# Kernel tuning notes

Hardware: AMD Instinct MI355X
Metric: run time of the kernel (lower is better)

Reference implementation:

```python
import math
import jax, jax.numpy as jnp
import numpy as np

EPS = 1e-5  # torch LayerNorm default
K_MA = 25   # moving-average kernel


def _layernorm(x, g, b):
    mu = x.mean(-1, keepdims=True)
    var = ((x - mu) ** 2).mean(-1, keepdims=True)
    return (x - mu) * jax.lax.rsqrt(var + EPS) * g + b


def _moving_avg(x, k=K_MA):
    # x: [B, L, C]; edge-replicate pad (k-1)//2 on both sides, avg window k, stride 1
    pad = (k - 1) // 2
    front = jnp.repeat(x[:, :1], pad, axis=1)
    back = jnp.repeat(x[:, -1:], pad, axis=1)
    xp = jnp.concatenate([front, x, back], axis=1)          # [B, L+2*pad, C]
    cs = jnp.cumsum(xp, axis=1)
    cs = jnp.concatenate([jnp.zeros_like(cs[:, :1]), cs], axis=1)
    return (cs[:, k:] - cs[:, :-k]) / k                     # [B, L, C]


def _autocorrelation(q, k, v, factor=1):
    # q,k,v: [B, L, H, D] -> FFT cross-correlation along time, top-k lag aggregation (inference path)
    B, L, H, D = q.shape
    qp = q.transpose(0, 2, 3, 1)                            # [B,H,D,L]
    kp = k.transpose(0, 2, 3, 1)
    vp = v.transpose(0, 2, 3, 1)
    qf = jnp.fft.rfft(qp, axis=-1)
    kf = jnp.fft.rfft(kp, axis=-1)
    corr = jnp.fft.irfft(qf * jnp.conj(kf), n=L, axis=-1)   # [B,H,D,L]

    top_k = int(factor * math.log(L))
    mean_corr = corr.mean(axis=(1, 2))                      # [B,L]
    weights, delay = jax.lax.top_k(mean_corr, top_k)        # [B,k]
    alpha = jax.nn.softmax(weights, axis=-1)                # [B,k]

    base = jnp.arange(L)
    agg = jnp.zeros_like(vp)
    for i in range(top_k):  # small static loop (top_k = 7)
        idx = (base[None, :] + delay[:, i:i + 1]) % L       # circular gather == roll by -delay
        gathered = jnp.take_along_axis(vp, idx[:, None, None, :], axis=-1)
        agg = agg + gathered * alpha[:, i][:, None, None, None]
    return agg.transpose(0, 3, 1, 2)                        # [B,L,H,D]


def _forward(x, Wq, Wk, Wv, Wo, bo, ln_g, ln_b, W1, W2, num_heads=16, factor=1):
    B, L, C = x.shape
    H = num_heads
    D = C // H
    xn = _layernorm(x, ln_g, ln_b)
    q = jnp.einsum('blc,oc->blo', xn, Wq).reshape(B, L, H, D)
    k = jnp.einsum('blc,oc->blo', xn, Wk).reshape(B, L, H, D)
    v = jnp.einsum('blc,oc->blo', xn, Wv).reshape(B, L, H, D)
    agg = _autocorrelation(q, k, v, factor=factor).reshape(B, L, C)
    attn_out = jnp.einsum('blc,oc->blo', agg, Wo) + bo
    x = x + attn_out
    x = x - _moving_avg(x)                                  # decomp1 seasonal part
    # FFN: 1x1 convs == linear layers, exact GELU (torch default)
    y = jax.nn.gelu(jnp.einsum('blc,hc->blh', x, W1), approximate=False)
    y = jnp.einsum('blh,ch->blc', y, W2)
    x = x + y
    x = x - _moving_avg(x)                                  # decomp2 seasonal part
    return x


def setup_inputs() -> dict:
    key = jax.random.key(0)
    ks = jax.random.split(key, 8)
    B, L, C = 8, 2048, 1024
    Hd = 4 * C
    s = 0.02
    return {
        'x': jax.random.normal(ks[0], (B, L, C), dtype=jnp.float32),
        'Wq': jax.random.normal(ks[1], (C, C), dtype=jnp.float32) * s,
        'Wk': jax.random.normal(ks[2], (C, C), dtype=jnp.float32) * s,
        'Wv': jax.random.normal(ks[3], (C, C), dtype=jnp.float32) * s,
        'Wo': jax.random.normal(ks[4], (C, C), dtype=jnp.float32) * s,
        'bo': jnp.zeros((C,), dtype=jnp.float32),
        'ln_g': jnp.ones((C,), dtype=jnp.float32),
        'ln_b': jnp.zeros((C,), dtype=jnp.float32),
        'W1': jax.random.normal(ks[5], (Hd, C), dtype=jnp.float32) * s,
        'W2': jax.random.normal(ks[6], (C, Hd), dtype=jnp.float32) * s,
    }


def reference(x, Wq, Wk, Wv, Wo, bo, ln_g, ln_b, W1, W2):
    return _forward(x, Wq, Wk, Wv, Wo, bo, ln_g, ln_b, W1, W2)
```

## Files before the change

kernel.cpp:

```cpp
#include <hip/hip_runtime.h>
#include <cstdint>
#include <cstddef>


typedef _Float16 half8 __attribute__((ext_vector_type(8)));
typedef _Float16 half4 __attribute__((ext_vector_type(4)));
typedef float floatx4 __attribute__((ext_vector_type(4)));

#define PI_F 3.14159265358979323846f
#define ZP32(i) ((i) + ((i) >> 5))

__device__ __forceinline__ void load_lds16(const void* g, void* l) {
  __builtin_amdgcn_global_load_lds((__attribute__((address_space(1))) void*)g,
                                   (__attribute__((address_space(3))) void*)l,
                                   16, 0, 0);
}

__device__ __forceinline__ float fast_gelu(float v) {
  float u = v * 0.70710678118654752f;
  float au = fabsf(u);
  float t = __builtin_amdgcn_rcpf(1.0f + 0.3275911f * au);
  float poly = t * (0.254829592f +
               t * (-0.284496736f +
               t * (1.421413741f +
               t * (-1.453152027f +
               t * 1.061405429f))));
  float e = __expf(-u * u);
  float erf_abs = 1.0f - poly * e;
  float erfv = copysignf(erf_abs, u);
  return 0.5f * v * (1.0f + erfv);
}


__global__ __launch_bounds__(256) void cvt_f16_kernel(const float* __restrict__ src,
                                                      _Float16* __restrict__ dst, int n4) {
  int i = blockIdx.x * 256 + threadIdx.x;
  if (i >= n4) return;
  float4 v = ((const float4*)src)[i];
  half4 h = {(_Float16)v.x, (_Float16)v.y, (_Float16)v.z, (_Float16)v.w};
  ((half4*)dst)[i] = h;
}

__global__ __launch_bounds__(256) void transpose_f16_kernel(const float* __restrict__ src,
                                                            _Float16* __restrict__ dst, int n) {
  __shared__ float tile[64][65];
  int j0 = blockIdx.y * 64, c0 = blockIdx.x * 64;
  int tr = threadIdx.x >> 4;
  int tc = threadIdx.x & 15;
#pragma unroll
  for (int rr = 0; rr < 64; rr += 16) {
    float4 v = *(const float4*)(src + (size_t)(j0 + tr + rr) * n + c0 + tc * 4);
    tile[tr + rr][tc * 4 + 0] = v.x;
    tile[tr + rr][tc * 4 + 1] = v.y;
    tile[tr + rr][tc * 4 + 2] = v.z;
    tile[tr + rr][tc * 4 + 3] = v.w;
  }
  __syncthreads();
#pragma unroll
  for (int rr = 0; rr < 64; rr += 16) {
    int c = tr + rr;
    half4 h = {(_Float16)tile[tc * 4 + 0][c], (_Float16)tile[tc * 4 + 1][c],
               (_Float16)tile[tc * 4 + 2][c], (_Float16)tile[tc * 4 + 3][c]};
    *(half4*)(dst + (size_t)(c0 + c) * n + j0 + tc * 4) = h;
  }
}

__global__ __launch_bounds__(256) void ln_kernel(const float* __restrict__ x,
                                                 const float* __restrict__ g,
                                                 const float* __restrict__ b,
                                                 _Float16* __restrict__ xn, int C) {
  int row = blockIdx.x;
  int t = threadIdx.x;
  const float4* xr = (const float4*)(x + (size_t)row * C);
  float4 v = xr[t];
  float s = v.x + v.y + v.z + v.w;
  float s2 = v.x * v.x + v.y * v.y + v.z * v.z + v.w * v.w;
  for (int o = 32; o > 0; o >>= 1) {
    s += __shfl_down(s, o, 64);
    s2 += __shfl_down(s2, o, 64);
  }
  __shared__ float red[8];
  int wave = t >> 6, lane = t & 63;
  if (lane == 0) { red[wave] = s; red[4 + wave] = s2; }
  __syncthreads();
  __shared__ float stats[2];
  if (t == 0) {
    float ts = red[0] + red[1] + red[2] + red[3];
    float ts2 = red[4] + red[5] + red[6] + red[7];
    float mu = ts / (float)C;
    float var = ts2 / (float)C - mu * mu;
    stats[0] = mu;
    stats[1] = 1.0f / sqrtf(var + 1e-5f);
  }
  __syncthreads();
  float mu = stats[0], rs = stats[1];
  float4 gv = ((const float4*)g)[t];
  float4 bv = ((const float4*)b)[t];
  half4 h = {(_Float16)((v.x - mu) * rs * gv.x + bv.x),
             (_Float16)((v.y - mu) * rs * gv.y + bv.y),
             (_Float16)((v.z - mu) * rs * gv.z + bv.z),
             (_Float16)((v.w - mu) * rs * gv.w + bv.w)};
  ((half4*)(xn + (size_t)row * C))[t] = h;
}

template <int EPI>
__global__ __launch_bounds__(512, 2) void gemm256_kernel(
    const _Float16* __restrict__ A, const _Float16* __restrict__ Bw,
    int M, int N, int K, int lda, int ldb,
    float* __restrict__ outf, _Float16* __restrict__ outh,
    const float* __restrict__ bias, const float* __restrict__ res) {
  __shared__ _Float16 lds[2][2][256 * 64];

  int tid = threadIdx.x;
  int lane = tid & 63;
  int wave = tid >> 6;
  int wm = wave >> 2;
  int wn = wave & 3;
  int ln15 = lane & 15, q4 = lane >> 4;
  int l3 = lane >> 3, l7 = lane & 7;

  int nwg = gridDim.x, orig = blockIdx.x;
  int wg = ((nwg & 7) == 0) ? ((orig & 7) * (nwg >> 3) + (orig >> 3)) : orig;
  int nbn = N >> 8;
  size_t m0 = (size_t)(wg / nbn) << 8;
  size_t n0 = (size_t)(wg % nbn) << 8;

  int sg0 = (q4 ^ l7) << 3;
  int sg1 = ((q4 + 4) ^ l7) << 3;

  floatx4 acc[8][4] = {};

  const _Float16* srcA = A + (m0 + 8 * wave + l3) * (size_t)lda + (size_t)((l7 ^ l3) * 8);
  const _Float16* srcB = Bw + (n0 + 8 * wave + l3) * (size_t)ldb + (size_t)((l7 ^ l3) * 8);
  char* ldsA0 = (char*)&lds[0][0][0] + wave * 1024;
  char* ldsB0 = (char*)&lds[0][1][0] + wave * 1024;

  load_lds16(srcB, ldsB0);
  load_lds16(srcB + (size_t)64 * ldb, ldsB0 + 1 * 8192);
  load_lds16(srcB + (size_t)128 * ldb, ldsB0 + 2 * 8192);
  load_lds16(srcB + (size_t)192 * ldb, ldsB0 + 3 * 8192);
  load_lds16(srcA, ldsA0);
  load_lds16(srcA + (size_t)128 * lda, ldsA0 + 2 * 8192);
  load_lds16(srcA + (size_t)64 * lda, ldsA0 + 1 * 8192);
  load_lds16(srcA + (size_t)192 * lda, ldsA0 + 3 * 8192);
  asm volatile("s_waitcnt vmcnt(2)" ::: "memory");
  __builtin_amdgcn_s_barrier();
  __builtin_amdgcn_sched_barrier(0);

  int nk = K >> 6;
  half8 bf[4][2], aA[2][2];

#define RD_B() _Pragma("unroll") for (int ni = 0; ni < 4; ++ni) {      \
    const _Float16* p_ = cB + ((wn * 64 + ni * 16 + ln15) << 6);       \
    bf[ni][0] = *(const half8*)(p_ + sg0);                             \
    bf[ni][1] = *(const half8*)(p_ + sg1); }
#define RD_A(mi) { const _Float16* p_ = cA + ((wm * 128 + (mi) * 16 + ln15) << 6); \
    aA[(mi) & 1][0] = *(const half8*)(p_ + sg0);                                   \
    aA[(mi) & 1][1] = *(const half8*)(p_ + sg1); }
#define MM(mi) _Pragma("unroll") for (int ni = 0; ni < 4; ++ni) {      \
    acc[mi][ni] = __builtin_amdgcn_mfma_f32_16x16x32_f16(aA[(mi) & 1][0], bf[ni][0], acc[mi][ni], 0, 0, 0); \
    acc[mi][ni] = __builtin_amdgcn_mfma_f32_16x16x32_f16(aA[(mi) & 1][1], bf[ni][1], acc[mi][ni], 0, 0, 0); }

#define PH_MID()                                            \
    __builtin_amdgcn_s_barrier();                           \
    asm volatile("s_waitcnt lgkmcnt(0)" ::: "memory");      \
    __builtin_amdgcn_sched_barrier(0);                      \
    __builtin_amdgcn_s_setprio(1);
#define PH_END()                                            \
    __builtin_amdgcn_s_setprio(0);                          \
    __builtin_amdgcn_s_barrier();                           \
    __builtin_amdgcn_sched_barrier(0);

  for (int t = 0; t < nk; ++t) {
    int cur = t & 1;
    const _Float16* cA = &lds[cur][0][0];
    const _Float16* cB = &lds[cur][1][0];
    const _Float16* As = srcA + (size_t)(t + 1) * 64;
    const _Float16* Bs = srcB + (size_t)(t + 1) * 64;
    char* stA = ldsA0 + (cur ^ 1) * 65536;
    char* stB = ldsB0 + (cur ^ 1) * 65536;
    bool pf = (t + 1 < nk);

    RD_B();
    RD_A(0); RD_A(1);
    if (pf) {
      load_lds16(Bs, stB);
      load_lds16(Bs + (size_t)64 * ldb, stB + 1 * 8192);
      load_lds16(Bs + (size_t)128 * ldb, stB + 2 * 8192);
    }
    PH_MID();
    MM(0); MM(1);
    PH_END();
    RD_A(2); RD_A(3);
    if (pf) {
      load_lds16(Bs + (size_t)192 * ldb, stB + 3 * 8192);
      load_lds16(As, stA);
      load_lds16(As + (size_t)128 * lda, stA + 2 * 8192);
    }
    PH_MID();
    MM(2); MM(3);
    __builtin_amdgcn_s_setprio(0);
    if (pf) {
      asm volatile("s_waitcnt vmcnt(6)" ::: "memory");
    } else {
      asm volatile("s_waitcnt vmcnt(0)" ::: "memory");
    }
    __builtin_amdgcn_s_barrier();
    __builtin_amdgcn_sched_barrier(0);
    RD_A(4); RD_A(5);
    if (pf) {
      load_lds16(As + (size_t)64 * lda, stA + 1 * 8192);
    }
    PH_MID();
    MM(4); MM(5);
    PH_END();
    RD_A(6); RD_A(7);
    if (pf) {
      load_lds16(As + (size_t)192 * lda, stA + 3 * 8192);
    }
    PH_MID();
    MM(6); MM(7);
    __builtin_amdgcn_s_setprio(0);
    asm volatile("s_waitcnt vmcnt(2)" ::: "memory");
    __builtin_amdgcn_s_barrier();
    __builtin_amdgcn_sched_barrier(0);
  }
#undef RD_B
#undef RD_A
#undef MM
#undef PH_MID
#undef PH_END

#pragma unroll
  for (int mi = 0; mi < 8; ++mi) {
#pragma unroll
    for (int ni = 0; ni < 4; ++ni) {
      floatx4 a4 = acc[mi][ni];
      size_t rowb = m0 + wm * 128 + mi * 16 + q4 * 4;
      size_t col = n0 + wn * 64 + ni * 16 + ln15;
      if (EPI == 5) {
        size_t b = rowb >> 11, l0 = rowb & 2047;
        half4 h = {(_Float16)a4[0], (_Float16)a4[1], (_Float16)a4[2], (_Float16)a4[3]};
        *(half4*)(outh + (((size_t)b * N + col) << 11) + l0) = h;
      } else {
#pragma unroll
        for (int r = 0; r < 4; ++r) {
          size_t idx = (rowb + r) * (size_t)N + col;
          float v = a4[r];
          if (EPI == 1) {
            outf[idx] = v + bias[col] + res[idx];
          } else if (EPI == 2) {
            outh[idx] = (_Float16)fast_gelu(v);
          } else if (EPI == 6) {
            outh[idx] = (_Float16)(v + res[idx]);
          } else if (EPI == 7) {
            float prev = (float)outh[idx];
            outh[idx] = (_Float16)(v + prev);
          } else {
            outh[idx] = (_Float16)v;
          }
        }
      }
    }
  }
}


#define CBFLY(ch, ia, ib, wr, wi) {                      \
    float ax_ = z[ch][ia].x, ay_ = z[ch][ia].y;          \
    float bx_ = z[ch][ib].x, by_ = z[ch][ib].y;          \
    float dx_ = ax_ - bx_, dy_ = ay_ - by_;              \
    z[ch][ia].x = ax_ + bx_; z[ch][ia].y = ay_ + by_;    \
    z[ch][ib].x = dx_ * (wr) - dy_ * (wi);               \
    z[ch][ib].y = dx_ * (wi) + dy_ * (wr); }
#define BFLY2(ia, ib, m) { float2 w_ = twl[ZP32(m)];     \
    CBFLY(0, ia, ib, w_.x, w_.y) CBFLY(1, ia, ib, w_.x, w_.y) }

__global__ __launch_bounds__(256) void corr_fft_kernel(const _Float16* __restrict__ F,
                                                       float* __restrict__ S) {
  __shared__ float2 Zs[2][2112];
  __shared__ float2 twl[1056];
  int tid = threadIdx.x;
  int b = blockIdx.x >> 9;
  int c0 = (blockIdx.x & 511) << 1;
  const _Float16* qb = F + ((size_t)(b * 2048 + c0) << 11);
  const _Float16* kb = F + ((size_t)(b * 2048 + 1024 + c0) << 11);

  float2 z[2][8];
#pragma unroll
  for (int j = 0; j < 8; ++j) {
    int p = tid + 256 * j;
    z[0][j] = make_float2((float)qb[p], (float)kb[p]);
    z[1][j] = make_float2((float)qb[2048 + p], (float)kb[2048 + p]);
  }
  for (int m = tid; m < 1024; m += 256) {
    float sn, cs;
    __sincosf(-PI_F * (float)m / 1024.0f, &sn, &cs);
    twl[ZP32(m)] = make_float2(cs, sn);
  }
  __syncthreads();

  BFLY2(0, 4, tid)
  BFLY2(1, 5, tid + 256)
  BFLY2(2, 6, tid + 512)
  BFLY2(3, 7, tid + 768)
  { float2 wA = twl[ZP32(tid << 1)], wB = twl[ZP32((tid + 256) << 1)];
    CBFLY(0, 0, 2, wA.x, wA.y) CBFLY(1, 0, 2, wA.x, wA.y)
    CBFLY(0, 1, 3, wB.x, wB.y) CBFLY(1, 1, 3, wB.x, wB.y)
    CBFLY(0, 4, 6, wA.x, wA.y) CBFLY(1, 4, 6, wA.x, wA.y)
    CBFLY(0, 5, 7, wB.x, wB.y) CBFLY(1, 5, 7, wB.x, wB.y) }
  { float2 wA = twl[ZP32(tid << 2)];
    CBFLY(0, 0, 1, wA.x, wA.y) CBFLY(1, 0, 1, wA.x, wA.y)
    CBFLY(0, 2, 3, wA.x, wA.y) CBFLY(1, 2, 3, wA.x, wA.y)
    CBFLY(0, 4, 5, wA.x, wA.y) CBFLY(1, 4, 5, wA.x, wA.y)
    CBFLY(0, 6, 7, wA.x, wA.y) CBFLY(1, 6, 7, wA.x, wA.y) }

#pragma unroll
  for (int j = 0; j < 8; ++j) {
    int p = tid + 256 * j;
    Zs[0][ZP32(p)] = z[0][j];
    Zs[1][ZP32(p)] = z[1][j];
  }
  __syncthreads();
  int t5 = tid & 31, hi1 = (tid >> 5) << 8;
#pragma unroll
  for (int j = 0; j < 8; ++j) {
    int p = hi1 + t5 + 32 * j;
    z[0][j] = Zs[0][ZP32(p)];
    z[1][j] = Zs[1][ZP32(p)];
  }

  BFLY2(0, 4, t5 << 3)
  BFLY2(1, 5, (t5 + 32) << 3)
  BFLY2(2, 6, (t5 + 64) << 3)
  BFLY2(3, 7, (t5 + 96) << 3)
  { float2 wA = twl[ZP32(t5 << 4)], wB = twl[ZP32((t5 + 32) << 4)];
    CBFLY(0, 0, 2, wA.x, wA.y) CBFLY(1, 0, 2, wA.x, wA.y)
    CBFLY(0, 1, 3, wB.x, wB.y) CBFLY(1, 1, 3, wB.x, wB.y)
    CBFLY(0, 4, 6, wA.x, wA.y) CBFLY(1, 4, 6, wA.x, wA.y)
    CBFLY(0, 5, 7, wB.x, wB.y) CBFLY(1, 5, 7, wB.x, wB.y) }
  { float2 wA = twl[ZP32(t5 << 5)];
    CBFLY(0, 0, 1, wA.x, wA.y) CBFLY(1, 0, 1, wA.x, wA.y)
    CBFLY(0, 2, 3, wA.x, wA.y) CBFLY(1, 2, 3, wA.x, wA.y)
    CBFLY(0, 4, 5, wA.x, wA.y) CBFLY(1, 4, 5, wA.x, wA.y)
    CBFLY(0, 6, 7, wA.x, wA.y) CBFLY(1, 6, 7, wA.x, wA.y) }

#pragma unroll
  for (int j = 0; j < 8; ++j) {
    int p = hi1 + t5 + 32 * j;
    Zs[0][ZP32(p)] = z[0][j];
    Zs[1][ZP32(p)] = z[1][j];
  }
  __syncthreads();
  int t3 = tid & 3, hi2 = (tid >> 2) << 5;
#pragma unroll
  for (int j = 0; j < 8; ++j) {
    int p = hi2 + t3 + 4 * j;
    z[0][j] = Zs[0][ZP32(p)];
    z[1][j] = Zs[1][ZP32(p)];
  }

  BFLY2(0, 4, t3 << 6)
  BFLY2(1, 5, (t3 + 4) << 6)
  BFLY2(2, 6, (t3 + 8) << 6)
  BFLY2(3, 7, (t3 + 12) << 6)
  { float2 wA = twl[ZP32(t3 << 7)], wB = twl[ZP32((t3 + 4) << 7)];
    CBFLY(0, 0, 2, wA.x, wA.y) CBFLY(1, 0, 2, wA.x, wA.y)
    CBFLY(0, 1, 3, wB.x, wB.y) CBFLY(1, 1, 3, wB.x, wB.y)
    CBFLY(0, 4, 6, wA.x, wA.y) CBFLY(1, 4, 6, wA.x, wA.y)
    CBFLY(0, 5, 7, wB.x, wB.y) CBFLY(1, 5, 7, wB.x, wB.y) }
  { float2 wA = twl[ZP32(t3 << 8)];
    CBFLY(0, 0, 1, wA.x, wA.y) CBFLY(1, 0, 1, wA.x, wA.y)
    CBFLY(0, 2, 3, wA.x, wA.y) CBFLY(1, 2, 3, wA.x, wA.y)
    CBFLY(0, 4, 5, wA.x, wA.y) CBFLY(1, 4, 5, wA.x, wA.y)
    CBFLY(0, 6, 7, wA.x, wA.y) CBFLY(1, 6, 7, wA.x, wA.y) }

#pragma unroll
  for (int j = 0; j < 8; ++j) {
    int p = hi2 + t3 + 4 * j;
    Zs[0][ZP32(p)] = z[0][j];
    Zs[1][ZP32(p)] = z[1][j];
  }
  __syncthreads();
#pragma unroll
  for (int j = 0; j < 8; ++j) {
    int p = (tid << 3) + j;
    z[0][j] = Zs[0][ZP32(p)];
    z[1][j] = Zs[1][ZP32(p)];
  }

  CBFLY(0, 0, 2, 1.0f, 0.0f) CBFLY(1, 0, 2, 1.0f, 0.0f)
  CBFLY(0, 1, 3, 0.0f, -1.0f) CBFLY(1, 1, 3, 0.0f, -1.0f)
  CBFLY(0, 4, 6, 1.0f, 0.0f) CBFLY(1, 4, 6, 1.0f, 0.0f)
  CBFLY(0, 5, 7, 0.0f, -1.0f) CBFLY(1, 5, 7, 0.0f, -1.0f)
  CBFLY(0, 0, 1, 1.0f, 0.0f) CBFLY(1, 0, 1, 1.0f, 0.0f)
  CBFLY(0, 2, 3, 1.0f, 0.0f) CBFLY(1, 2, 3, 1.0f, 0.0f)
  CBFLY(0, 4, 5, 1.0f, 0.0f) CBFLY(1, 4, 5, 1.0f, 0.0f)
  CBFLY(0, 6, 7, 1.0f, 0.0f) CBFLY(1, 6, 7, 1.0f, 0.0f)

#pragma unroll
  for (int j = 0; j < 8; ++j) {
    int p = (tid << 3) + j;
    Zs[0][ZP32(p)] = z[0][j];
    Zs[1][ZP32(p)] = z[1][j];
  }
  __syncthreads();
  float* Sb = S + (size_t)blockIdx.x * 2050;
  for (int f = tid; f <= 1024; f += 256) {
    int rf = __brev((unsigned)f) >> 21;
    int rmf = __brev((unsigned)((2048 - f) & 2047)) >> 21;
    float pr = 0.f, pim = 0.f;
#pragma unroll
    for (int ch = 0; ch < 2; ++ch) {
      float2 zf = Zs[ch][ZP32(rf)], zm = Zs[ch][ZP32(rmf)];
      float Qr = 0.5f * (zf.x + zm.x), Qi = 0.5f * (zf.y - zm.y);
      float Kr = 0.5f * (zf.y + zm.y), Ki = -0.5f * (zf.x - zm.x);
      pr += Qr * Kr + Qi * Ki;
      pim += Qi * Kr - Qr * Ki;
    }
    Sb[2 * f] = pr;
    Sb[2 * f + 1] = pim;
  }
}

__global__ __launch_bounds__(256) void spec_reduce_kernel(const float* __restrict__ Sbig,
                                                          float* __restrict__ S8) {
  int f = blockIdx.x * 256 + threadIdx.x;
  int sc = blockIdx.y;
  int b = blockIdx.z;
  if (f >= 2050) return;
  const float* src = Sbig + ((size_t)b * 512 + (size_t)sc * 64) * 2050 + f;
  float s = 0.f;
  for (int i = 0; i < 64; ++i) s += src[(size_t)i * 2050];
  S8[((size_t)b * 8 + sc) * 2050 + f] = s;
}

__global__ __launch_bounds__(256) void corr_topk_kernel(const float* __restrict__ S,
                                                        int* __restrict__ delays,
                                                        float* __restrict__ alphas,
                                                        int C, int L) {
  __shared__ float2 W[2048];
  __shared__ float mc[2048];
  __shared__ float rv[4];
  __shared__ int ri[4];
  __shared__ float swv[7];
  __shared__ int sdi[7];
  int b = blockIdx.x, tid = threadIdx.x;
  const float* Sb = S + (size_t)b * 8 * 2050;
  for (int f = tid; f < 2048; f += 256) {
    int ff = f <= 1024 ? f : 2048 - f;
    float re = 0.f, im = 0.f;
    for (int s = 0; s < 8; ++s) {
      re += Sb[s * 2050 + 2 * ff];
      im += Sb[s * 2050 + 2 * ff + 1];
    }
    W[f] = make_float2(re, f <= 1024 ? -im : im);
  }
  __syncthreads();
  for (int sh = 10; sh >= 0; --sh) {
    int s = 1 << sh;
    for (int j = tid; j < 1024; j += 256) {
      int t = j & (s - 1);
      int i0 = ((j >> sh) << (sh + 1)) | t;
      int i1 = i0 + s;
      float2 a = W[i0], bb = W[i1];
      float ang = -PI_F * (float)t / (float)s;
      float sn, cs;
      __sincosf(ang, &sn, &cs);
      float2 d = make_float2(a.x - bb.x, a.y - bb.y);
      W[i0] = make_float2(a.x + bb.x, a.y + bb.y);
      W[i1] = make_float2(d.x * cs - d.y * sn, d.x * sn + d.y * cs);
    }
    __syncthreads();
  }
  float inv = 1.0f / ((float)C * (float)L);
  for (int t = tid; t < 2048; t += 256) mc[t] = W[__brev((unsigned)t) >> 21].x * inv;
  __syncthreads();
  int wv = tid >> 6, lane = tid & 63;
  for (int it = 0; it < 7; ++it) {
    float bvv = -1e30f;
    int bi = 0;
    for (int e = tid * 8; e < tid * 8 + 8; ++e) {
      float v = mc[e];
      if (v > bvv) { bvv = v; bi = e; }
    }
    for (int o = 32; o > 0; o >>= 1) {
      float ov = __shfl_down(bvv, o, 64);
      int oi = __shfl_down(bi, o, 64);
      if (ov > bvv || (ov == bvv && oi < bi)) { bvv = ov; bi = oi; }
    }
    if (lane == 0) { rv[wv] = bvv; ri[wv] = bi; }
    __syncthreads();
    if (tid == 0) {
      float fv = rv[0];
      int fi = ri[0];
      for (int w2 = 1; w2 < 4; ++w2)
        if (rv[w2] > fv || (rv[w2] == fv && ri[w2] < fi)) { fv = rv[w2]; fi = ri[w2]; }
      swv[it] = fv;
      sdi[it] = fi;
      mc[fi] = -1e30f;
    }
    __syncthreads();
  }
  if (tid == 0) {
    float mx = swv[0];
    for (int i = 1; i < 7; ++i) mx = fmaxf(mx, swv[i]);
    float e[7], s = 0.f;
    for (int i = 0; i < 7; ++i) { e[i] = expf(swv[i] - mx); s += e[i]; }
    for (int i = 0; i < 7; ++i) {
      alphas[b * 7 + i] = e[i] / s;
      delays[b * 7 + i] = sdi[i];
    }
  }
}

__global__ __launch_bounds__(256) void agg_kernel(const _Float16* __restrict__ v,
                                                  const int* __restrict__ delays,
                                                  const float* __restrict__ alphas,
                                                  _Float16* __restrict__ agg,
                                                  int L, int C) {
  int bt = blockIdx.x;
  int b = bt >> 11, t = bt & 2047;
  int tid = threadIdx.x;
  const _Float16* vb = v + (size_t)b * L * C;
  float ax = 0.f, ay = 0.f, az = 0.f, aw = 0.f;
#pragma unroll
  for (int i = 0; i < 7; ++i) {
    int d = delays[b * 7 + i];
    float a = alphas[b * 7 + i];
    int src = t + d;
    if (src >= L) src -= L;
    half4 x = ((const half4*)(vb + (size_t)src * C))[tid];
    ax += a * (float)x.x; ay += a * (float)x.y;
    az += a * (float)x.z; aw += a * (float)x.w;
  }
  half4 h = {(_Float16)ax, (_Float16)ay, (_Float16)az, (_Float16)aw};
  ((half4*)(agg + (size_t)bt * C))[tid] = h;
}

template <int WRITE_H>
__global__ __launch_bounds__(256) void decomp_kernel(const float* __restrict__ xin,
                                                     float* __restrict__ xout,
                                                     _Float16* __restrict__ xh,
                                                     int L, int C) {
  int c = blockIdx.x * 256 + threadIdx.x;
  int t0 = blockIdx.y * 128;
  int b = blockIdx.z;
  const float* xb = xin + (size_t)b * L * C + c;
  float sum = 0.f;
  for (int j = t0 - 12; j <= t0 + 12; ++j) {
    int jc = j < 0 ? 0 : (j > L - 1 ? L - 1 : j);
    sum += xb[(size_t)jc * C];
  }
  for (int t = t0; t < t0 + 128; ++t) {
    float xv = xb[(size_t)t * C];
    float o = xv - sum * (1.0f / 25.0f);
    size_t oidx = ((size_t)b * L + t) * C + c;
    xout[oidx] = o;
    if (WRITE_H) xh[oidx] = (_Float16)o;
    int nj = t + 13; if (nj > L - 1) nj = L - 1;
    int oj = t - 12; if (oj < 0) oj = 0;
    sum += xb[(size_t)nj * C] - xb[(size_t)oj * C];
  }
}

__global__ __launch_bounds__(256) void decomp_h_kernel(const _Float16* __restrict__ xin,
                                                       float* __restrict__ xout,
                                                       int L, int C) {
  int c = blockIdx.x * 256 + threadIdx.x;
  int t0 = blockIdx.y * 128;
  int b = blockIdx.z;
  const _Float16* xb = xin + (size_t)b * L * C + c;
  float sum = 0.f;
  for (int j = t0 - 12; j <= t0 + 12; ++j) {
    int jc = j < 0 ? 0 : (j > L - 1 ? L - 1 : j);
    sum += (float)xb[(size_t)jc * C];
  }
  for (int t = t0; t < t0 + 128; ++t) {
    float xv = (float)xb[(size_t)t * C];
    float o = xv - sum * (1.0f / 25.0f);
    xout[((size_t)b * L + t) * C + c] = o;
    int nj = t + 13; if (nj > L - 1) nj = L - 1;
    int oj = t - 12; if (oj < 0) oj = 0;
    sum += (float)xb[(size_t)nj * C] - (float)xb[(size_t)oj * C];
  }
}

extern "C" void kernel_launch(void* const* d_in, const int* in_sizes, int n_in,
                              void* d_out, int out_size, void* d_ws, size_t ws_size,
                              hipStream_t stream) {
  const float* x = (const float*)d_in[0];
  const float* Wq = (const float*)d_in[1];
  const float* Wk = (const float*)d_in[2];
  const float* Wv = (const float*)d_in[3];
  const float* Wo = (const float*)d_in[4];
  const float* bo = (const float*)d_in[5];
  const float* lng = (const float*)d_in[6];
  const float* lnb = (const float*)d_in[7];
  const float* W1 = (const float*)d_in[8];
  const float* W2 = (const float*)d_in[9];
  float* out = (float*)d_out;

  const int B = 8, L = 2048, C = 1024, HD = 4096;
  const int M = B * L;

  char* ws = (char*)d_ws;
  size_t off = 0;
  auto alloc = [&](size_t bytes) -> void* {
    void* p = ws + off;
    off = (off + bytes + 255) & ~(size_t)255;
    return p;
  };
  _Float16* wqkh = (_Float16*)alloc((size_t)2 * C * C * 2);
  _Float16* wvoh = (_Float16*)alloc((size_t)C * C * 2);
  _Float16* w1h = (_Float16*)alloc((size_t)HD * C * 2);
  _Float16* w2h = (_Float16*)alloc((size_t)C * HD * 2);
  float* S8 = (float*)alloc((size_t)B * 8 * 2050 * 4);
  int* dl = (int*)alloc(B * 7 * 4);
  float* al = (float*)alloc(B * 7 * 4);
  _Float16* xn = (_Float16*)alloc((size_t)M * C * 2);
  _Float16* qkh = (_Float16*)alloc((size_t)M * 2 * C * 2);
  _Float16* vh = (_Float16*)alloc((size_t)4096 * 2050 * 4);
  (void)ws_size; (void)in_sizes; (void)n_in; (void)out_size;

  _Float16* wvT = vh;
  _Float16* woh = vh + (size_t)C * C;
  float* Sbig = (float*)vh;
  _Float16* aggh = vh;
  float* x1 = (float*)qkh;
  _Float16* x2h = xn;
  float* x2 = out;
  _Float16* hid2 = qkh;
  _Float16* x3h = vh;

  cvt_f16_kernel<<<(C * C / 4 + 255) / 256, 256, 0, stream>>>(Wq, wqkh, C * C / 4);
  cvt_f16_kernel<<<(C * C / 4 + 255) / 256, 256, 0, stream>>>(Wk, wqkh + (size_t)C * C, C * C / 4);
  cvt_f16_kernel<<<(C * C / 4 + 255) / 256, 256, 0, stream>>>(Wo, woh, C * C / 4);
  transpose_f16_kernel<<<dim3(16, 16), 256, 0, stream>>>(Wv, wvT, C);
  cvt_f16_kernel<<<(HD * C / 4 + 255) / 256, 256, 0, stream>>>(W1, w1h, HD * C / 4);
  cvt_f16_kernel<<<(HD * C / 4 + 255) / 256, 256, 0, stream>>>(W2, w2h, HD * C / 4);
  gemm256_kernel<4><<<16, 512, 0, stream>>>(woh, wvT, C, C, C, C, C,
                                            nullptr, wvoh, nullptr, nullptr);
  ln_kernel<<<M, 256, 0, stream>>>(x, lng, lnb, xn, C);
  gemm256_kernel<5><<<(M / 256) * (2 * C / 256), 512, 0, stream>>>(
      xn, wqkh, M, 2 * C, C, C, C, nullptr, qkh, nullptr, nullptr);
  corr_fft_kernel<<<B * (C / 2), 256, 0, stream>>>(qkh, Sbig);
  spec_reduce_kernel<<<dim3(9, 8, 8), 256, 0, stream>>>(Sbig, S8);
  corr_topk_kernel<<<B, 256, 0, stream>>>(S8, dl, al, C, L);
  agg_kernel<<<B * L, 256, 0, stream>>>(xn, dl, al, aggh, L, C);
  gemm256_kernel<1><<<(M / 256) * (C / 256), 512, 0, stream>>>(
      aggh, wvoh, M, C, C, C, C, x1, nullptr, bo, x);
  decomp_kernel<1><<<dim3(C / 256, L / 128, B), 256, 0, stream>>>(x1, x2, x2h, L, C);
  for (int ci = 0; ci < 2; ++ci) {
    gemm256_kernel<2><<<(M / 256) * (2048 / 256), 512, 0, stream>>>(
        x2h, w1h + (size_t)ci * 2048 * C, M, 2048, C, C, C,
        nullptr, hid2, nullptr, nullptr);
    if (ci == 0) {
      gemm256_kernel<6><<<(M / 256) * (C / 256), 512, 0, stream>>>(
          hid2, w2h, M, C, 2048, 2048, HD, nullptr, x3h, nullptr, x2);
    } else {
      gemm256_kernel<7><<<(M / 256) * (C / 256), 512, 0, stream>>>(
          hid2, w2h + 2048, M, C, 2048, 2048, HD, nullptr, x3h, nullptr, nullptr);
    }
  }
  decomp_h_kernel<<<dim3(C / 256, L / 128, B), 256, 0, stream>>>(x3h, out, L, C);
}
```

Before: 833.2 us.

## Stage GEMM epilogues through LDS for vectorized stores and keep residuals in fp16

The GEMM epilogues for the GELU, bias+residual and accumulate variants now write the tile to LDS first. They then read it back row-contiguously so each thread issues 16-byte half8 global loads and stores instead of scattered 2-byte accesses. The attention-output GEMM now writes fp16 instead of fp32, and the first decomposition reads and writes fp16 only, dropping the fp32 x2 copy. The MLP residual now comes from the fp16 x2h. This cuts global memory traffic and improves coalescing, at the cost of an extra LDS round trip and barrier, plus more rounding in the residual path.

```diff
diff --git a/kernel.cpp b/kernel.cpp
--- a/kernel.cpp
+++ b/kernel.cpp
@@ -108,7 +108,8 @@
     const _Float16* __restrict__ A, const _Float16* __restrict__ Bw,
     int M, int N, int K, int lda, int ldb,
     float* __restrict__ outf, _Float16* __restrict__ outh,
-    const float* __restrict__ bias, const float* __restrict__ res) {
+    const float* __restrict__ bias, const float* __restrict__ res,
+    const _Float16* __restrict__ resh) {
   __shared__ _Float16 lds[2][2][256 * 64];
 
   int tid = threadIdx.x;
@@ -231,33 +232,75 @@
 #undef PH_MID
 #undef PH_END
 
-#pragma unroll
-  for (int mi = 0; mi < 8; ++mi) {
-#pragma unroll
-    for (int ni = 0; ni < 4; ++ni) {
-      floatx4 a4 = acc[mi][ni];
-      size_t rowb = m0 + wm * 128 + mi * 16 + q4 * 4;
-      size_t col = n0 + wn * 64 + ni * 16 + ln15;
-      if (EPI == 5) {
-        size_t b = rowb >> 11, l0 = rowb & 2047;
-        half4 h = {(_Float16)a4[0], (_Float16)a4[1], (_Float16)a4[2], (_Float16)a4[3]};
-        *(half4*)(outh + (((size_t)b * N + col) << 11) + l0) = h;
-      } else {
+  if (EPI == 2 || EPI == 7 || EPI == 8 || EPI == 9) {
+    _Float16* eb = (_Float16*)&lds[0][0][0];
+#pragma unroll
+    for (int mi = 0; mi < 8; ++mi) {
+#pragma unroll
+      for (int ni = 0; ni < 4; ++ni) {
+        floatx4 a4 = acc[mi][ni];
+        int erow = wm * 128 + mi * 16 + q4 * 4;
+        int ecol = wn * 64 + ni * 16 + ln15;
 #pragma unroll
         for (int r = 0; r < 4; ++r) {
-          size_t idx = (rowb + r) * (size_t)N + col;
           float v = a4[r];
-          if (EPI == 1) {
-            outf[idx] = v + bias[col] + res[idx];
-          } else if (EPI == 2) {
-            outh[idx] = (_Float16)fast_gelu(v);
-          } else if (EPI == 6) {
-            outh[idx] = (_Float16)(v + res[idx]);
-          } else if (EPI == 7) {
-            float prev = (float)outh[idx];
-            outh[idx] = (_Float16)(v + prev);
-          } else {
-            outh[idx] = (_Float16)v;
+          if (EPI == 2) v = fast_gelu(v);
+          eb[(size_t)(erow + r) * 256 + ecol] = (_Float16)v;
+        }
+      }
+    }
+    __syncthreads();
+    int baser = (tid >> 6) * 32 + (((tid & 63) >> 5) << 4);
+    int ecol2 = (tid & 31) << 3;
+    float4 bv0, bv1;
+    if (EPI == 9) {
+      bv0 = *(const float4*)(bias + n0 + ecol2);
+      bv1 = *(const float4*)(bias + n0 + ecol2 + 4);
+    }
+#pragma unroll
+    for (int jr = 0; jr < 16; ++jr) {
+      int row = baser + jr;
+      half8 hv = *(const half8*)(eb + (size_t)row * 256 + ecol2);
+      size_t gidx = (m0 + row) * (size_t)N + n0 + ecol2;
+      if (EPI == 7) {
+        half8 pv = *(const half8*)(outh + gidx);
+#pragma unroll
+        for (int k = 0; k < 8; ++k) hv[k] = (_Float16)((float)hv[k] + (float)pv[k]);
+      } else if (EPI == 8) {
+        half8 pv = *(const half8*)(resh + gidx);
+#pragma unroll
+        for (int k = 0; k < 8; ++k) hv[k] = (_Float16)((float)hv[k] + (float)pv[k]);
+      } else if (EPI == 9) {
+        float4 rv0 = *(const float4*)(res + gidx);
+        float4 rv1 = *(const float4*)(res + gidx + 4);
+        hv[0] = (_Float16)((float)hv[0] + bv0.x + rv0.x);
+        hv[1] = (_Float16)((float)hv[1] + bv0.y + rv0.y);
+        hv[2] = (_Float16)((float)hv[2] + bv0.z + rv0.z);
+        hv[3] = (_Float16)((float)hv[3] + bv0.w + rv0.w);
+        hv[4] = (_Float16)((float)hv[4] + bv1.x + rv1.x);
+        hv[5] = (_Float16)((float)hv[5] + bv1.y + rv1.y);
+        hv[6] = (_Float16)((float)hv[6] + bv1.z + rv1.z);
+        hv[7] = (_Float16)((float)hv[7] + bv1.w + rv1.w);
+      }
+      *(half8*)(outh + gidx) = hv;
+    }
+  } else {
+#pragma unroll
+    for (int mi = 0; mi < 8; ++mi) {
+#pragma unroll
+      for (int ni = 0; ni < 4; ++ni) {
+        floatx4 a4 = acc[mi][ni];
+        size_t rowb = m0 + wm * 128 + mi * 16 + q4 * 4;
+        size_t col = n0 + wn * 64 + ni * 16 + ln15;
+        if (EPI == 5) {
+          size_t b = rowb >> 11, l0 = rowb & 2047;
+          half4 h = {(_Float16)a4[0], (_Float16)a4[1], (_Float16)a4[2], (_Float16)a4[3]};
+          *(half4*)(outh + (((size_t)b * N + col) << 11) + l0) = h;
+        } else {
+#pragma unroll
+          for (int r = 0; r < 4; ++r) {
+            size_t idx = (rowb + r) * (size_t)N + col;
+            outh[idx] = (_Float16)a4[r];
           }
         }
       }
@@ -538,29 +581,25 @@
   ((half4*)(agg + (size_t)bt * C))[tid] = h;
 }
 
-template <int WRITE_H>
-__global__ __launch_bounds__(256) void decomp_kernel(const float* __restrict__ xin,
-                                                     float* __restrict__ xout,
-                                                     _Float16* __restrict__ xh,
-                                                     int L, int C) {
+__global__ __launch_bounds__(256) void decomp_hh_kernel(const _Float16* __restrict__ xin,
+                                                        _Float16* __restrict__ xout,
+                                                        int L, int C) {
   int c = blockIdx.x * 256 + threadIdx.x;
   int t0 = blockIdx.y * 128;
   int b = blockIdx.z;
-  const float* xb = xin + (size_t)b * L * C + c;
+  const _Float16* xb = xin + (size_t)b * L * C + c;
   float sum = 0.f;
   for (int j = t0 - 12; j <= t0 + 12; ++j) {
     int jc = j < 0 ? 0 : (j > L - 1 ? L - 1 : j);
-    sum += xb[(size_t)jc * C];
+    sum += (float)xb[(size_t)jc * C];
   }
   for (int t = t0; t < t0 + 128; ++t) {
-    float xv = xb[(size_t)t * C];
+    float xv = (float)xb[(size_t)t * C];
     float o = xv - sum * (1.0f / 25.0f);
-    size_t oidx = ((size_t)b * L + t) * C + c;
-    xout[oidx] = o;
-    if (WRITE_H) xh[oidx] = (_Float16)o;
+    xout[((size_t)b * L + t) * C + c] = (_Float16)o;
     int nj = t + 13; if (nj > L - 1) nj = L - 1;
     int oj = t - 12; if (oj < 0) oj = 0;
-    sum += xb[(size_t)nj * C] - xb[(size_t)oj * C];
+    sum += (float)xb[(size_t)nj * C] - (float)xb[(size_t)oj * C];
   }
 }
 
@@ -627,9 +666,8 @@
   _Float16* woh = vh + (size_t)C * C;
   float* Sbig = (float*)vh;
   _Float16* aggh = vh;
-  float* x1 = (float*)qkh;
+  _Float16* x1h = qkh;
   _Float16* x2h = xn;
-  float* x2 = out;
   _Float16* hid2 = qkh;
   _Float16* x3h = vh;
 
@@ -640,27 +678,27 @@
   cvt_f16_kernel<<<(HD * C / 4 + 255) / 256, 256, 0, stream>>>(W1, w1h, HD * C / 4);
   cvt_f16_kernel<<<(HD * C / 4 + 255) / 256, 256, 0, stream>>>(W2, w2h, HD * C / 4);
   gemm256_kernel<4><<<16, 512, 0, stream>>>(woh, wvT, C, C, C, C, C,
-                                            nullptr, wvoh, nullptr, nullptr);
+                                            nullptr, wvoh, nullptr, nullptr, nullptr);
   ln_kernel<<<M, 256, 0, stream>>>(x, lng, lnb, xn, C);
   gemm256_kernel<5><<<(M / 256) * (2 * C / 256), 512, 0, stream>>>(
-      xn, wqkh, M, 2 * C, C, C, C, nullptr, qkh, nullptr, nullptr);
+      xn, wqkh, M, 2 * C, C, C, C, nullptr, qkh, nullptr, nullptr, nullptr);
   corr_fft_kernel<<<B * (C / 2), 256, 0, stream>>>(qkh, Sbig);
   spec_reduce_kernel<<<dim3(9, 8, 8), 256, 0, stream>>>(Sbig, S8);
   corr_topk_kernel<<<B, 256, 0, stream>>>(S8, dl, al, C, L);
   agg_kernel<<<B * L, 256, 0, stream>>>(xn, dl, al, aggh, L, C);
-  gemm256_kernel<1><<<(M / 256) * (C / 256), 512, 0, stream>>>(
-      aggh, wvoh, M, C, C, C, C, x1, nullptr, bo, x);
-  decomp_kernel<1><<<dim3(C / 256, L / 128, B), 256, 0, stream>>>(x1, x2, x2h, L, C);
+  gemm256_kernel<9><<<(M / 256) * (C / 256), 512, 0, stream>>>(
+      aggh, wvoh, M, C, C, C, C, nullptr, x1h, bo, x, nullptr);
+  decomp_hh_kernel<<<dim3(C / 256, L / 128, B), 256, 0, stream>>>(x1h, x2h, L, C);
   for (int ci = 0; ci < 2; ++ci) {
     gemm256_kernel<2><<<(M / 256) * (2048 / 256), 512, 0, stream>>>(
         x2h, w1h + (size_t)ci * 2048 * C, M, 2048, C, C, C,
-        nullptr, hid2, nullptr, nullptr);
+        nullptr, hid2, nullptr, nullptr, nullptr);
     if (ci == 0) {
-      gemm256_kernel<6><<<(M / 256) * (C / 256), 512, 0, stream>>>(
-          hid2, w2h, M, C, 2048, 2048, HD, nullptr, x3h, nullptr, x2);
+      gemm256_kernel<8><<<(M / 256) * (C / 256), 512, 0, stream>>>(
+          hid2, w2h, M, C, 2048, 2048, HD, nullptr, x3h, nullptr, nullptr, x2h);
     } else {
       gemm256_kernel<7><<<(M / 256) * (C / 256), 512, 0, stream>>>(
-          hid2, w2h + 2048, M, C, 2048, 2048, HD, nullptr, x3h, nullptr, nullptr);
+          hid2, w2h + 2048, M, C, 2048, 2048, HD, nullptr, x3h, nullptr, nullptr, nullptr);
     }
   }
   decomp_h_kernel<<<dim3(C / 256, L / 128, B), 256, 0, stream>>>(x3h, out, L, C);
```

Result: faster. 792.2 us (-4.9%).
